# Performance work log

Measured on AMD Instinct MI355X. Metric: run time of the kernel, lower is better.

## Reference

```python
import jax, jax.numpy as jnp
import numpy as np

BN_EPS = 1e-5

def setup_inputs() -> dict:
    key = jax.random.key(0)
    ks = jax.random.split(key, 4)
    N, C, T, V, H = 32, 64, 512, 25, 3
    x = jax.random.normal(ks[0], (N, C, T, V), dtype=jnp.float32)
    A = jax.random.normal(ks[1], (H, V, V), dtype=jnp.float32)
    # per-head 1x1 conv weights (conv_branch_init-like small std) and biases
    W = jax.random.normal(ks[2], (H, C, C), dtype=jnp.float32) * 0.05
    b = jax.random.normal(ks[3], (H, C), dtype=jnp.float32) * 0.05
    gamma = jnp.ones((C,), dtype=jnp.float32)
    beta = jnp.zeros((C,), dtype=jnp.float32)
    return {"x": x, "A": A, "W": W, "b": b, "gamma": gamma, "beta": beta}

def reference(x, A, W, b, gamma, beta):
    # x: [N,C,T,V], A: [H,V,V], W: [H,Cout,Cin], b: [H,Cout]
    # per-head graph conv: z_h[n,c,t,v] = sum_u A[h,v,u] * x[n,c,t,u]
    z = jnp.einsum('hvu,nctu->hnctv', A, x)
    # per-head 1x1 conv (channel mix) then sum over heads; biases sum too
    out = jnp.einsum('hoc,hnctv->notv', W, z) + b.sum(axis=0)[None, :, None, None]
    # BatchNorm2d (training-mode batch stats, biased variance) over (N,T,V)
    mean = out.mean(axis=(0, 2, 3), keepdims=True)
    var = out.var(axis=(0, 2, 3), keepdims=True)
    out = gamma[None, :, None, None] * (out - mean) * jax.lax.rsqrt(var + BN_EPS) \
          + beta[None, :, None, None]
    # residual (in_channels == out_channels -> identity down) + ReLU
    return jnp.maximum(out + x, 0.0)
```

## Files before the change

kernel.cpp:

```cpp
#include <hip/hip_runtime.h>
#include <hip/hip_bf16.h>

#define N_DIM 32
#define C_DIM 64
#define T_DIM 512
#define V_DIM 25
#define H_DIM 3
#define TT 8
#define NBLK1 2048
#define NTGRP 2048
#define NTV (N_DIM * T_DIM * V_DIM)
#define NTOT (N_DIM * C_DIM * T_DIM * V_DIM)
#define XPITCH 76
#define XROWS 208
#define TILE_SH 1792
#define SITER 13
#define BN_EPS 1e-5f

typedef float f32x4 __attribute__((ext_vector_type(4)));
typedef short bf16x8 __attribute__((ext_vector_type(8)));
typedef short s16x4 __attribute__((ext_vector_type(4)));

__device__ __forceinline__ short f2bf(float f) {
    __hip_bfloat16 h = __float2bfloat16(f);
    return __builtin_bit_cast(short, h);
}
__device__ __forceinline__ float bf2f(short s) {
    return __uint_as_float(((unsigned)(unsigned short)s) << 16);
}

__device__ __forceinline__ bf16x8 ld_bf8(const short* p) {
    s16x4 a = *(const s16x4*)p;
    s16x4 b = *(const s16x4*)(p + 4);
    bf16x8 r;
    r[0] = a[0]; r[1] = a[1]; r[2] = a[2]; r[3] = a[3];
    r[4] = b[0]; r[5] = b[1]; r[6] = b[2]; r[7] = b[3];
    return r;
}

__global__ __launch_bounds__(256) void gcn_pack(
    const float* __restrict__ A, const float* __restrict__ W,
    short* __restrict__ wpack, short* __restrict__ apack)
{
    const int b   = blockIdx.x;
    const int tid = threadIdx.x;
    const int l15 = tid & 15, hi = (tid >> 4) & 3, w = tid >> 6;
    if (b < 6) {
        int h = b >> 1, s = b & 1;
        const float* wp = W + h * 4096 + (16 * w + l15) * 64 + s * 32 + hi * 8;
        bf16x8 f;
        #pragma unroll
        for (int i = 0; i < 8; ++i) f[i] = f2bf(wp[i]);
        *(bf16x8*)(wpack + ((size_t)b * 256 + tid) * 8) = f;
    } else {
        int bb = b - 6, h = bb >> 1, vt = bb & 1;
        int v = vt * 16 + l15;
        bf16x8 f;
        #pragma unroll
        for (int i = 0; i < 8; ++i) {
            int u = hi * 8 + i;
            f[i] = (v < 25 && u < 25) ? f2bf(A[h * 625 + v * 25 + u]) : (short)0;
        }
        *(bf16x8*)(apack + ((size_t)bb * 256 + tid) * 8) = f;
    }
}

__device__ __forceinline__ void stage_load(float (&fr)[SITER][4],
                                           const float* __restrict__ xg, int tid)
{
    #pragma unroll
    for (int k = 0; k < SITER; ++k) {
        int e = tid + k * 256;
        if (k < SITER - 1 || e < 3200) {
            int cg = e / 200, tu = e - cg * 200;
            const float* p = xg + cg * 51200 + tu;
            fr[k][0] = p[0];
            fr[k][1] = p[12800];
            fr[k][2] = p[25600];
            fr[k][3] = p[38400];
        }
    }
}
__device__ __forceinline__ void stage_write(const float (&fr)[SITER][4],
                                            short* __restrict__ dst, int tid)
{
    #pragma unroll
    for (int k = 0; k < SITER; ++k) {
        int e = tid + k * 256;
        if (k < SITER - 1 || e < 3200) {
            int cg = e / 200, tu = e - cg * 200;
            s16x4 v; v[0] = f2bf(fr[k][0]); v[1] = f2bf(fr[k][1]);
                     v[2] = f2bf(fr[k][2]); v[3] = f2bf(fr[k][3]);
            *(s16x4*)&dst[tu * XPITCH + 4 * cg] = v;
        }
    }
}

template <int SCR>
__global__ __launch_bounds__(256, 4) void gcn_pass1(
    const float* __restrict__ x, const float* __restrict__ A,
    const float* __restrict__ W, const short* __restrict__ wpack,
    const short* __restrict__ apack, void* __restrict__ scratch_,
    float* __restrict__ partial)
{
    __shared__ __align__(16) short x_sT[XROWS * XPITCH];

    const int bid  = blockIdx.x;
    const int n    = bid >> 6;
    const int tgrp = bid & 63;
    const int tid  = threadIdx.x;
    const int lane = tid & 63;
    const int w    = tid >> 6;
    const int l15  = lane & 15;
    const int hi   = lane >> 4;

    {
        float fr[SITER][4];
        stage_load(fr, x + (size_t)n * 819200 + tgrp * (TT * 25), tid);
        for (int e = tid; e < 304; e += 256)
            ((int*)&x_sT[200 * XPITCH])[e] = 0;
        stage_write(fr, &x_sT[0], tid);
    }

    bf16x8 wf[H_DIM][2], af[H_DIM][2];
    if constexpr (SCR) {
        #pragma unroll
        for (int h = 0; h < H_DIM; ++h)
            #pragma unroll
            for (int s = 0; s < 2; ++s) {
                wf[h][s] = *(const bf16x8*)(wpack + ((h * 2 + s) * 256 + tid) * 8);
                af[h][s] = *(const bf16x8*)(apack + ((h * 2 + s) * 256 + tid) * 8);
            }
    } else {
        #pragma unroll
        for (int h = 0; h < H_DIM; ++h)
            #pragma unroll
            for (int s = 0; s < 2; ++s) {
                const f32x4* wp = (const f32x4*)(W + h * 4096 + (16 * w + l15) * 64
                                                 + s * 32 + hi * 8);
                f32x4 lo = wp[0], hv = wp[1];
                bf16x8 f;
                #pragma unroll
                for (int i = 0; i < 4; ++i) { f[i] = f2bf(lo[i]); f[4+i] = f2bf(hv[i]); }
                wf[h][s] = f;
                int v = s * 16 + l15;
                bf16x8 g;
                #pragma unroll
                for (int i = 0; i < 8; ++i) {
                    int u = hi * 8 + i;
                    g[i] = (v < 25 && u < 25) ? f2bf(A[h * 625 + v * 25 + u]) : (short)0;
                }
                af[h][s] = g;
            }
    }
    __syncthreads();

    const int ubase = ((l15 >> 2) * 8) + (l15 & 3);
    const int o_glob = 16 * w + l15;
    float s_tot = 0.f, q_tot = 0.f;

    #pragma unroll 2
    for (int t = 0; t < TT; ++t) {
        const short* xr0 = &x_sT[(t * 25 + ubase + 0) * XPITCH + hi * 8];
        const short* xr1 = &x_sT[(t * 25 + ubase + 4) * XPITCH + hi * 8];
        const bf16x8 xf00 = ld_bf8(xr0), xf01 = ld_bf8(xr0 + 32);
        const bf16x8 xf10 = ld_bf8(xr1), xf11 = ld_bf8(xr1 + 32);

        f32x4 acc2[2] = {f32x4{0.f,0.f,0.f,0.f}, f32x4{0.f,0.f,0.f,0.f}};

        #pragma unroll
        for (int h = 0; h < H_DIM; ++h) {
            f32x4 y0 = {0.f,0.f,0.f,0.f}, y1 = {0.f,0.f,0.f,0.f};
            y0 = __builtin_amdgcn_mfma_f32_16x16x32_bf16(xf00, wf[h][0], y0, 0,0,0);
            y0 = __builtin_amdgcn_mfma_f32_16x16x32_bf16(xf01, wf[h][1], y0, 0,0,0);
            y1 = __builtin_amdgcn_mfma_f32_16x16x32_bf16(xf10, wf[h][0], y1, 0,0,0);
            y1 = __builtin_amdgcn_mfma_f32_16x16x32_bf16(xf11, wf[h][1], y1, 0,0,0);
            bf16x8 yf;
            #pragma unroll
            for (int j = 0; j < 4; ++j) yf[j] = f2bf(y0[j]);
            #pragma unroll
            for (int j = 0; j < 4; ++j) yf[4 + j] = f2bf(y1[j]);
            acc2[0] = __builtin_amdgcn_mfma_f32_16x16x32_bf16(af[h][0], yf, acc2[0], 0,0,0);
            acc2[1] = __builtin_amdgcn_mfma_f32_16x16x32_bf16(af[h][1], yf, acc2[1], 0,0,0);
        }

        if (SCR) {
            short* base = (short*)scratch_
                        + ((size_t)(n * 512 + tgrp * TT + t)) * TILE_SH;
            s16x4 p0; p0[0]=f2bf(acc2[0][0]); p0[1]=f2bf(acc2[0][1]);
                      p0[2]=f2bf(acc2[0][2]); p0[3]=f2bf(acc2[0][3]);
            *(s16x4*)(base + w * 256 + hi * 64 + l15 * 4) = p0;
            if (hi < 3) {
                s16x4 p1; p1[0]=f2bf(acc2[1][0]); p1[1]=f2bf(acc2[1][1]);
                          p1[2]=f2bf(acc2[1][2]); p1[3]=f2bf(acc2[1][3]);
                *(s16x4*)(base + 1024 + w * 192 + hi * 64 + l15 * 4) = p1;
            }
        } else {
            float* op = (float*)scratch_
                      + ((size_t)(n * 64 + o_glob) * 512 + tgrp * TT + t) * 25;
            #pragma unroll
            for (int j = 0; j < 4; ++j) op[hi * 4 + j] = acc2[0][j];
            if (hi < 2) {
                #pragma unroll
                for (int j = 0; j < 4; ++j) op[16 + hi * 4 + j] = acc2[1][j];
            } else if (hi == 2) {
                op[24] = acc2[1][0];
            }
        }

        float s = acc2[0][0] + acc2[0][1] + acc2[0][2] + acc2[0][3];
        float qq = fmaf(acc2[0][0], acc2[0][0], fmaf(acc2[0][1], acc2[0][1],
                   fmaf(acc2[0][2], acc2[0][2], acc2[0][3] * acc2[0][3])));
        if (hi < 2) {
            #pragma unroll
            for (int j = 0; j < 4; ++j) {
                float v1 = acc2[1][j]; s += v1; qq = fmaf(v1, v1, qq);
            }
        } else if (hi == 2) {
            float v1 = acc2[1][0]; s += v1; qq = fmaf(v1, v1, qq);
        }
        s_tot += s; q_tot += qq;
    }

    s_tot += __shfl_xor(s_tot, 16); q_tot += __shfl_xor(q_tot, 16);
    s_tot += __shfl_xor(s_tot, 32); q_tot += __shfl_xor(q_tot, 32);
    if (hi == 0) {
        partial[bid * 128 + o_glob]      = s_tot;
        partial[bid * 128 + 64 + o_glob] = q_tot;
    }
}

__global__ __launch_bounds__(256) void gcn_stats(
    const float* __restrict__ partial, float* __restrict__ stats)
{
    const int o = blockIdx.x;
    const int tid = threadIdx.x;
    float s = 0.f, q = 0.f;
    for (int blk = tid; blk < NBLK1; blk += 256) {
        s += partial[blk * 128 + o];
        q += partial[blk * 128 + 64 + o];
    }
    __shared__ float rs[256], rq[256];
    rs[tid] = s; rq[tid] = q;
    __syncthreads();
    for (int off = 128; off > 0; off >>= 1) {
        if (tid < off) { rs[tid] += rs[tid + off]; rq[tid] += rq[tid + off]; }
        __syncthreads();
    }
    if (tid == 0) {
        float mean = rs[0] / (float)NTV;
        float var  = rq[0] / (float)NTV - mean * mean;
        stats[o]      = mean;
        stats[64 + o] = rsqrtf(var + BN_EPS);
    }
}

__device__ __forceinline__ int swz16(int chunk) {
    return chunk ^ ((chunk >> 3) & 7);
}

__global__ __launch_bounds__(256) void gcn_finalize_b(
    const float* __restrict__ x, const float* __restrict__ gamma,
    const float* __restrict__ beta, const float* __restrict__ stats,
    const short* __restrict__ scr, float* __restrict__ out)
{
    __shared__ __align__(16) short tl_s[8 * TILE_SH];
    const int bid  = blockIdx.x;
    const int n    = bid >> 6;
    const int tgrp = bid & 63;
    const int tid  = threadIdx.x;

    const int4* src = (const int4*)(scr + (size_t)bid * 8 * TILE_SH);
    int4* dst4 = (int4*)tl_s;
    #pragma unroll
    for (int k = 0; k < 7; ++k) {
        int i = tid + k * 256;
        dst4[swz16(i)] = src[i];
    }
    __syncthreads();

    const size_t obase = (size_t)n * 819200 + (size_t)tgrp * 200;
    #pragma unroll
    for (int k = 0; k < 13; ++k) {
        int fi = tid + k * 256;
        if (fi < 3200) {
            int o  = fi / 50;
            int p  = (fi - o * 50) * 4;
            int tl = p / 25;
            int v0 = p - tl * 25;
            float gm = gamma[o] * stats[64 + o];
            float bc = beta[o] - gm * stats[o];
            size_t gidx = obase + (size_t)o * 12800 + p;
            float4 xv = *(const float4*)(x + gidx);
            float r[4];
            #pragma unroll
            for (int j = 0; j < 4; ++j) {
                int vv = v0 + j, tt = tl;
                if (vv >= 25) { vv -= 25; tt += 1; }
                int off = (vv < 16)
                    ? ((o >> 4) * 256 + (vv >> 2) * 64 + (o & 15) * 4 + (vv & 3))
                    : (1024 + (o >> 4) * 192 + ((vv - 16) >> 2) * 64
                       + (o & 15) * 4 + (vv & 3));
                int raw = tt * TILE_SH + off;
                int adr = swz16(raw >> 3) * 8 + (raw & 7);
                float pv = bf2f(tl_s[adr]);
                r[j] = fmaxf(fmaf(gm, pv, bc) + (&xv.x)[j], 0.f);
            }
            float4 o4; o4.x = r[0]; o4.y = r[1]; o4.z = r[2]; o4.w = r[3];
            *(float4*)(out + gidx) = o4;
        }
    }
}

__global__ __launch_bounds__(256) void gcn_finalize_f(
    const float* __restrict__ x, const float* __restrict__ gamma,
    const float* __restrict__ beta, const float* __restrict__ stats,
    float* __restrict__ out)
{
    const int total4 = NTOT / 4;
    for (int i = blockIdx.x * blockDim.x + threadIdx.x; i < total4;
         i += gridDim.x * blockDim.x) {
        int chan = ((i * 4) / (T_DIM * V_DIM)) & 63;
        float4 p  = ((const float4*)out)[i];
        float4 xv = ((const float4*)x)[i];
        float m = stats[chan], r = stats[64 + chan];
        float g = gamma[chan] * r;
        float bc = beta[chan] - g * m;
        p.x = fmaxf(fmaf(g, p.x, bc) + xv.x, 0.f);
        p.y = fmaxf(fmaf(g, p.y, bc) + xv.y, 0.f);
        p.z = fmaxf(fmaf(g, p.z, bc) + xv.z, 0.f);
        p.w = fmaxf(fmaf(g, p.w, bc) + xv.w, 0.f);
        ((float4*)out)[i] = p;
    }
}

extern "C" void kernel_launch(void* const* d_in, const int* in_sizes, int n_in,
                              void* d_out, int out_size, void* d_ws, size_t ws_size,
                              hipStream_t stream) {
    const float* x     = (const float*)d_in[0];
    const float* A     = (const float*)d_in[1];
    const float* W     = (const float*)d_in[2];
    const float* gamma = (const float*)d_in[4];
    const float* beta  = (const float*)d_in[5];
    float* out = (float*)d_out;

    const size_t scr_bytes   = (size_t)N_DIM * T_DIM * TILE_SH * 2;
    const size_t part_bytes  = (size_t)NBLK1 * 128 * 4;
    const size_t stats_bytes = 512;
    const size_t pack_bytes  = 2 * 6 * 256 * 8 * 2;

    if (ws_size >= scr_bytes + part_bytes + stats_bytes + pack_bytes) {
        short* scr     = (short*)d_ws;
        float* partial = (float*)((char*)d_ws + scr_bytes);
        float* stats   = partial + NBLK1 * 128;
        short* wpack   = (short*)((char*)d_ws + scr_bytes + part_bytes + stats_bytes);
        short* apack   = wpack + 6 * 256 * 8;

        gcn_pack<<<12, 256, 0, stream>>>(A, W, wpack, apack);
        gcn_pass1<1><<<NBLK1, 256, 0, stream>>>(x, A, W, wpack, apack,
                                                (void*)scr, partial);
        gcn_stats<<<64, 256, 0, stream>>>(partial, stats);
        gcn_finalize_b<<<NTGRP, 256, 0, stream>>>(x, gamma, beta, stats, scr, out);
    } else {
        float* partial = (float*)d_ws;
        float* stats   = partial + NBLK1 * 128;
        gcn_pass1<0><<<NBLK1, 256, 0, stream>>>(x, A, W, nullptr, nullptr,
                                                (void*)out, partial);
        gcn_stats<<<64, 256, 0, stream>>>(partial, stats);
        gcn_finalize_f<<<2048, 256, 0, stream>>>(x, gamma, beta, stats, out);
    }
}
```

Measured before the change: 89.99 us.

## Recompute graph conv in finalize instead of round-tripping bf16 scratch

The first pass now only computes the per-channel sum and sum-of-squares, without writing the pre-BN activations to a bf16 scratch buffer. A new fused kernel re-stages x, recomputes both MFMA stages with swapped operand order so output rows map to channels, and applies the folded BN scale/shift, residual and ReLU directly. The BN scale and shift are now folded once in the stats kernel. This trades the scratch write and read traffic for a second read of x and a repeat of the matrix work; the final stores are scalar and partly masked rather than float4.

```diff
diff --git a/kernel.cpp b/kernel.cpp
--- a/kernel.cpp
+++ b/kernel.cpp
@@ -8,12 +8,10 @@
 #define H_DIM 3
 #define TT 8
 #define NBLK1 2048
-#define NTGRP 2048
 #define NTV (N_DIM * T_DIM * V_DIM)
 #define NTOT (N_DIM * C_DIM * T_DIM * V_DIM)
 #define XPITCH 76
 #define XROWS 208
-#define TILE_SH 1792
 #define SITER 13
 #define BN_EPS 1e-5f
 
@@ -24,9 +22,6 @@
 __device__ __forceinline__ short f2bf(float f) {
     __hip_bfloat16 h = __float2bfloat16(f);
     return __builtin_bit_cast(short, h);
-}
-__device__ __forceinline__ float bf2f(short s) {
-    return __uint_as_float(((unsigned)(unsigned short)s) << 16);
 }
 
 __device__ __forceinline__ bf16x8 ld_bf8(const short* p) {
@@ -96,12 +91,9 @@
     }
 }
 
-template <int SCR>
-__global__ __launch_bounds__(256, 4) void gcn_pass1(
-    const float* __restrict__ x, const float* __restrict__ A,
-    const float* __restrict__ W, const short* __restrict__ wpack,
-    const short* __restrict__ apack, void* __restrict__ scratch_,
-    float* __restrict__ partial)
+__global__ __launch_bounds__(256, 4) void gcn_statsconv(
+    const float* __restrict__ x, const short* __restrict__ wpack,
+    const short* __restrict__ apack, float* __restrict__ partial)
 {
     __shared__ __align__(16) short x_sT[XROWS * XPITCH];
 
@@ -123,36 +115,13 @@
     }
 
     bf16x8 wf[H_DIM][2], af[H_DIM][2];
-    if constexpr (SCR) {
-        #pragma unroll
-        for (int h = 0; h < H_DIM; ++h)
-            #pragma unroll
-            for (int s = 0; s < 2; ++s) {
-                wf[h][s] = *(const bf16x8*)(wpack + ((h * 2 + s) * 256 + tid) * 8);
-                af[h][s] = *(const bf16x8*)(apack + ((h * 2 + s) * 256 + tid) * 8);
-            }
-    } else {
-        #pragma unroll
-        for (int h = 0; h < H_DIM; ++h)
-            #pragma unroll
-            for (int s = 0; s < 2; ++s) {
-                const f32x4* wp = (const f32x4*)(W + h * 4096 + (16 * w + l15) * 64
-                                                 + s * 32 + hi * 8);
-                f32x4 lo = wp[0], hv = wp[1];
-                bf16x8 f;
-                #pragma unroll
-                for (int i = 0; i < 4; ++i) { f[i] = f2bf(lo[i]); f[4+i] = f2bf(hv[i]); }
-                wf[h][s] = f;
-                int v = s * 16 + l15;
-                bf16x8 g;
-                #pragma unroll
-                for (int i = 0; i < 8; ++i) {
-                    int u = hi * 8 + i;
-                    g[i] = (v < 25 && u < 25) ? f2bf(A[h * 625 + v * 25 + u]) : (short)0;
-                }
-                af[h][s] = g;
-            }
-    }
+    #pragma unroll
+    for (int h = 0; h < H_DIM; ++h)
+        #pragma unroll
+        for (int s = 0; s < 2; ++s) {
+            wf[h][s] = *(const bf16x8*)(wpack + ((h * 2 + s) * 256 + tid) * 8);
+            af[h][s] = *(const bf16x8*)(apack + ((h * 2 + s) * 256 + tid) * 8);
+        }
     __syncthreads();
 
     const int ubase = ((l15 >> 2) * 8) + (l15 & 3);
@@ -184,30 +153,6 @@
             acc2[1] = __builtin_amdgcn_mfma_f32_16x16x32_bf16(af[h][1], yf, acc2[1], 0,0,0);
         }
 
-        if (SCR) {
-            short* base = (short*)scratch_
-                        + ((size_t)(n * 512 + tgrp * TT + t)) * TILE_SH;
-            s16x4 p0; p0[0]=f2bf(acc2[0][0]); p0[1]=f2bf(acc2[0][1]);
-                      p0[2]=f2bf(acc2[0][2]); p0[3]=f2bf(acc2[0][3]);
-            *(s16x4*)(base + w * 256 + hi * 64 + l15 * 4) = p0;
-            if (hi < 3) {
-                s16x4 p1; p1[0]=f2bf(acc2[1][0]); p1[1]=f2bf(acc2[1][1]);
-                          p1[2]=f2bf(acc2[1][2]); p1[3]=f2bf(acc2[1][3]);
-                *(s16x4*)(base + 1024 + w * 192 + hi * 64 + l15 * 4) = p1;
-            }
-        } else {
-            float* op = (float*)scratch_
-                      + ((size_t)(n * 64 + o_glob) * 512 + tgrp * TT + t) * 25;
-            #pragma unroll
-            for (int j = 0; j < 4; ++j) op[hi * 4 + j] = acc2[0][j];
-            if (hi < 2) {
-                #pragma unroll
-                for (int j = 0; j < 4; ++j) op[16 + hi * 4 + j] = acc2[1][j];
-            } else if (hi == 2) {
-                op[24] = acc2[1][0];
-            }
-        }
-
         float s = acc2[0][0] + acc2[0][1] + acc2[0][2] + acc2[0][3];
         float qq = fmaf(acc2[0][0], acc2[0][0], fmaf(acc2[0][1], acc2[0][1],
                    fmaf(acc2[0][2], acc2[0][2], acc2[0][3] * acc2[0][3])));
@@ -231,7 +176,8 @@
 }
 
 __global__ __launch_bounds__(256) void gcn_stats(
-    const float* __restrict__ partial, float* __restrict__ stats)
+    const float* __restrict__ partial, const float* __restrict__ gamma,
+    const float* __restrict__ beta, float* __restrict__ stats2)
 {
     const int o = blockIdx.x;
     const int tid = threadIdx.x;
@@ -250,71 +196,205 @@
     if (tid == 0) {
         float mean = rs[0] / (float)NTV;
         float var  = rq[0] / (float)NTV - mean * mean;
-        stats[o]      = mean;
-        stats[64 + o] = rsqrtf(var + BN_EPS);
-    }
-}
-
-__device__ __forceinline__ int swz16(int chunk) {
-    return chunk ^ ((chunk >> 3) & 7);
-}
-
-__global__ __launch_bounds__(256) void gcn_finalize_b(
-    const float* __restrict__ x, const float* __restrict__ gamma,
-    const float* __restrict__ beta, const float* __restrict__ stats,
-    const short* __restrict__ scr, float* __restrict__ out)
-{
-    __shared__ __align__(16) short tl_s[8 * TILE_SH];
+        float gm = gamma[o] * rsqrtf(var + BN_EPS);
+        stats2[o]      = gm;
+        stats2[64 + o] = beta[o] - gm * mean;
+    }
+}
+
+__global__ __launch_bounds__(256, 4) void gcn_fused(
+    const float* __restrict__ x, const short* __restrict__ wpack,
+    const short* __restrict__ apack, const float* __restrict__ stats2,
+    float* __restrict__ out)
+{
+    __shared__ __align__(16) short x_sT[XROWS * XPITCH];
+
     const int bid  = blockIdx.x;
     const int n    = bid >> 6;
     const int tgrp = bid & 63;
     const int tid  = threadIdx.x;
-
-    const int4* src = (const int4*)(scr + (size_t)bid * 8 * TILE_SH);
-    int4* dst4 = (int4*)tl_s;
-    #pragma unroll
-    for (int k = 0; k < 7; ++k) {
-        int i = tid + k * 256;
-        dst4[swz16(i)] = src[i];
+    const int lane = tid & 63;
+    const int w    = tid >> 6;
+    const int l15  = lane & 15;
+    const int hi   = lane >> 4;
+
+    {
+        float fr[SITER][4];
+        stage_load(fr, x + (size_t)n * 819200 + tgrp * (TT * 25), tid);
+        for (int e = tid; e < 304; e += 256)
+            ((int*)&x_sT[200 * XPITCH])[e] = 0;
+        stage_write(fr, &x_sT[0], tid);
+    }
+
+    bf16x8 wf[H_DIM][2], af[H_DIM][2];
+    #pragma unroll
+    for (int h = 0; h < H_DIM; ++h)
+        #pragma unroll
+        for (int s = 0; s < 2; ++s) {
+            wf[h][s] = *(const bf16x8*)(wpack + ((h * 2 + s) * 256 + tid) * 8);
+            af[h][s] = *(const bf16x8*)(apack + ((h * 2 + s) * 256 + tid) * 8);
+        }
+
+    float gm[4], bc[4];
+    #pragma unroll
+    for (int j = 0; j < 4; ++j) {
+        int o = 16 * w + hi * 4 + j;
+        gm[j] = stats2[o];
+        bc[j] = stats2[64 + o];
     }
     __syncthreads();
 
-    const size_t obase = (size_t)n * 819200 + (size_t)tgrp * 200;
-    #pragma unroll
-    for (int k = 0; k < 13; ++k) {
-        int fi = tid + k * 256;
-        if (fi < 3200) {
-            int o  = fi / 50;
-            int p  = (fi - o * 50) * 4;
-            int tl = p / 25;
-            int v0 = p - tl * 25;
-            float gm = gamma[o] * stats[64 + o];
-            float bc = beta[o] - gm * stats[o];
-            size_t gidx = obase + (size_t)o * 12800 + p;
-            float4 xv = *(const float4*)(x + gidx);
-            float r[4];
+    const int ubase = ((l15 >> 2) * 8) + (l15 & 3);
+    const size_t rb0 = ((size_t)(n * 64 + 16 * w + hi * 4) * 512
+                        + (size_t)tgrp * TT) * 25;
+
+    #pragma unroll 2
+    for (int t = 0; t < TT; ++t) {
+        const short* xr0 = &x_sT[(t * 25 + ubase + 0) * XPITCH + hi * 8];
+        const short* xr1 = &x_sT[(t * 25 + ubase + 4) * XPITCH + hi * 8];
+        const bf16x8 xf00 = ld_bf8(xr0), xf01 = ld_bf8(xr0 + 32);
+        const bf16x8 xf10 = ld_bf8(xr1), xf11 = ld_bf8(xr1 + 32);
+
+        f32x4 accA = {0.f,0.f,0.f,0.f};
+        f32x4 accB = {0.f,0.f,0.f,0.f};
+
+        #pragma unroll
+        for (int h = 0; h < H_DIM; ++h) {
+            f32x4 y0 = {0.f,0.f,0.f,0.f}, y1 = {0.f,0.f,0.f,0.f};
+            y0 = __builtin_amdgcn_mfma_f32_16x16x32_bf16(xf00, wf[h][0], y0, 0,0,0);
+            y0 = __builtin_amdgcn_mfma_f32_16x16x32_bf16(xf01, wf[h][1], y0, 0,0,0);
+            y1 = __builtin_amdgcn_mfma_f32_16x16x32_bf16(xf10, wf[h][0], y1, 0,0,0);
+            y1 = __builtin_amdgcn_mfma_f32_16x16x32_bf16(xf11, wf[h][1], y1, 0,0,0);
+            bf16x8 yf;
+            #pragma unroll
+            for (int j = 0; j < 4; ++j) yf[j] = f2bf(y0[j]);
+            #pragma unroll
+            for (int j = 0; j < 4; ++j) yf[4 + j] = f2bf(y1[j]);
+            accA = __builtin_amdgcn_mfma_f32_16x16x32_bf16(yf, af[h][0], accA, 0,0,0);
+            accB = __builtin_amdgcn_mfma_f32_16x16x32_bf16(yf, af[h][1], accB, 0,0,0);
+        }
+
+        #pragma unroll
+        for (int j = 0; j < 4; ++j) {
+            size_t idx = rb0 + (size_t)j * 12800 + (size_t)t * 25 + l15;
+            float xv = x[idx];
+            out[idx] = fmaxf(fmaf(gm[j], accA[j], bc[j]) + xv, 0.f);
+            if (l15 < 9) {
+                float xv1 = x[idx + 16];
+                out[idx + 16] = fmaxf(fmaf(gm[j], accB[j], bc[j]) + xv1, 0.f);
+            }
+        }
+    }
+}
+
+__global__ __launch_bounds__(256, 4) void gcn_pass1_f(
+    const float* __restrict__ x, const float* __restrict__ A,
+    const float* __restrict__ W, float* __restrict__ out_pre,
+    float* __restrict__ partial)
+{
+    __shared__ __align__(16) short x_sT[XROWS * XPITCH];
+
+    const int bid  = blockIdx.x;
+    const int n    = bid >> 6;
+    const int tgrp = bid & 63;
+    const int tid  = threadIdx.x;
+    const int lane = tid & 63;
+    const int w    = tid >> 6;
+    const int l15  = lane & 15;
+    const int hi   = lane >> 4;
+
+    {
+        float fr[SITER][4];
+        stage_load(fr, x + (size_t)n * 819200 + tgrp * (TT * 25), tid);
+        for (int e = tid; e < 304; e += 256)
+            ((int*)&x_sT[200 * XPITCH])[e] = 0;
+        stage_write(fr, &x_sT[0], tid);
+    }
+
+    bf16x8 wf[H_DIM][2], af[H_DIM][2];
+    #pragma unroll
+    for (int h = 0; h < H_DIM; ++h)
+        #pragma unroll
+        for (int s = 0; s < 2; ++s) {
+            const f32x4* wp = (const f32x4*)(W + h * 4096 + (16 * w + l15) * 64
+                                             + s * 32 + hi * 8);
+            f32x4 lo = wp[0], hv = wp[1];
+            bf16x8 f;
+            #pragma unroll
+            for (int i = 0; i < 4; ++i) { f[i] = f2bf(lo[i]); f[4+i] = f2bf(hv[i]); }
+            wf[h][s] = f;
+            int v = s * 16 + l15;
+            bf16x8 g;
+            #pragma unroll
+            for (int i = 0; i < 8; ++i) {
+                int u = hi * 8 + i;
+                g[i] = (v < 25 && u < 25) ? f2bf(A[h * 625 + v * 25 + u]) : (short)0;
+            }
+            af[h][s] = g;
+        }
+    __syncthreads();
+
+    const int ubase = ((l15 >> 2) * 8) + (l15 & 3);
+    const int o_glob = 16 * w + l15;
+    float s_tot = 0.f, q_tot = 0.f;
+
+    for (int t = 0; t < TT; ++t) {
+        const short* xr0 = &x_sT[(t * 25 + ubase + 0) * XPITCH + hi * 8];
+        const short* xr1 = &x_sT[(t * 25 + ubase + 4) * XPITCH + hi * 8];
+        const bf16x8 xf00 = ld_bf8(xr0), xf01 = ld_bf8(xr0 + 32);
+        const bf16x8 xf10 = ld_bf8(xr1), xf11 = ld_bf8(xr1 + 32);
+
+        f32x4 acc2[2] = {f32x4{0.f,0.f,0.f,0.f}, f32x4{0.f,0.f,0.f,0.f}};
+        #pragma unroll
+        for (int h = 0; h < H_DIM; ++h) {
+            f32x4 y0 = {0.f,0.f,0.f,0.f}, y1 = {0.f,0.f,0.f,0.f};
+            y0 = __builtin_amdgcn_mfma_f32_16x16x32_bf16(xf00, wf[h][0], y0, 0,0,0);
+            y0 = __builtin_amdgcn_mfma_f32_16x16x32_bf16(xf01, wf[h][1], y0, 0,0,0);
+            y1 = __builtin_amdgcn_mfma_f32_16x16x32_bf16(xf10, wf[h][0], y1, 0,0,0);
+            y1 = __builtin_amdgcn_mfma_f32_16x16x32_bf16(xf11, wf[h][1], y1, 0,0,0);
+            bf16x8 yf;
+            #pragma unroll
+            for (int j = 0; j < 4; ++j) yf[j] = f2bf(y0[j]);
+            #pragma unroll
+            for (int j = 0; j < 4; ++j) yf[4 + j] = f2bf(y1[j]);
+            acc2[0] = __builtin_amdgcn_mfma_f32_16x16x32_bf16(af[h][0], yf, acc2[0], 0,0,0);
+            acc2[1] = __builtin_amdgcn_mfma_f32_16x16x32_bf16(af[h][1], yf, acc2[1], 0,0,0);
+        }
+
+        float* op = out_pre + ((size_t)(n * 64 + o_glob) * 512 + tgrp * TT + t) * 25;
+        #pragma unroll
+        for (int j = 0; j < 4; ++j) op[hi * 4 + j] = acc2[0][j];
+        if (hi < 2) {
+            #pragma unroll
+            for (int j = 0; j < 4; ++j) op[16 + hi * 4 + j] = acc2[1][j];
+        } else if (hi == 2) {
+            op[24] = acc2[1][0];
+        }
+
+        float s = acc2[0][0] + acc2[0][1] + acc2[0][2] + acc2[0][3];
+        float qq = fmaf(acc2[0][0], acc2[0][0], fmaf(acc2[0][1], acc2[0][1],
+                   fmaf(acc2[0][2], acc2[0][2], acc2[0][3] * acc2[0][3])));
+        if (hi < 2) {
             #pragma unroll
             for (int j = 0; j < 4; ++j) {
-                int vv = v0 + j, tt = tl;
-                if (vv >= 25) { vv -= 25; tt += 1; }
-                int off = (vv < 16)
-                    ? ((o >> 4) * 256 + (vv >> 2) * 64 + (o & 15) * 4 + (vv & 3))
-                    : (1024 + (o >> 4) * 192 + ((vv - 16) >> 2) * 64
-                       + (o & 15) * 4 + (vv & 3));
-                int raw = tt * TILE_SH + off;
-                int adr = swz16(raw >> 3) * 8 + (raw & 7);
-                float pv = bf2f(tl_s[adr]);
-                r[j] = fmaxf(fmaf(gm, pv, bc) + (&xv.x)[j], 0.f);
+                float v1 = acc2[1][j]; s += v1; qq = fmaf(v1, v1, qq);
             }
-            float4 o4; o4.x = r[0]; o4.y = r[1]; o4.z = r[2]; o4.w = r[3];
-            *(float4*)(out + gidx) = o4;
-        }
+        } else if (hi == 2) {
+            float v1 = acc2[1][0]; s += v1; qq = fmaf(v1, v1, qq);
+        }
+        s_tot += s; q_tot += qq;
+    }
+
+    s_tot += __shfl_xor(s_tot, 16); q_tot += __shfl_xor(q_tot, 16);
+    s_tot += __shfl_xor(s_tot, 32); q_tot += __shfl_xor(q_tot, 32);
+    if (hi == 0) {
+        partial[bid * 128 + o_glob]      = s_tot;
+        partial[bid * 128 + 64 + o_glob] = q_tot;
     }
 }
 
 __global__ __launch_bounds__(256) void gcn_finalize_f(
-    const float* __restrict__ x, const float* __restrict__ gamma,
-    const float* __restrict__ beta, const float* __restrict__ stats,
+    const float* __restrict__ x, const float* __restrict__ stats2,
     float* __restrict__ out)
 {
     const int total4 = NTOT / 4;
@@ -323,9 +403,7 @@
         int chan = ((i * 4) / (T_DIM * V_DIM)) & 63;
         float4 p  = ((const float4*)out)[i];
         float4 xv = ((const float4*)x)[i];
-        float m = stats[chan], r = stats[64 + chan];
-        float g = gamma[chan] * r;
-        float bc = beta[chan] - g * m;
+        float g = stats2[chan], bc = stats2[64 + chan];
         p.x = fmaxf(fmaf(g, p.x, bc) + xv.x, 0.f);
         p.y = fmaxf(fmaf(g, p.y, bc) + xv.y, 0.f);
         p.z = fmaxf(fmaf(g, p.z, bc) + xv.z, 0.f);
@@ -344,29 +422,23 @@
     const float* beta  = (const float*)d_in[5];
     float* out = (float*)d_out;
 
-    const size_t scr_bytes   = (size_t)N_DIM * T_DIM * TILE_SH * 2;
     const size_t part_bytes  = (size_t)NBLK1 * 128 * 4;
     const size_t stats_bytes = 512;
     const size_t pack_bytes  = 2 * 6 * 256 * 8 * 2;
 
-    if (ws_size >= scr_bytes + part_bytes + stats_bytes + pack_bytes) {
-        short* scr     = (short*)d_ws;
-        float* partial = (float*)((char*)d_ws + scr_bytes);
-        float* stats   = partial + NBLK1 * 128;
-        short* wpack   = (short*)((char*)d_ws + scr_bytes + part_bytes + stats_bytes);
-        short* apack   = wpack + 6 * 256 * 8;
-
+    float* partial = (float*)d_ws;
+    float* stats2  = partial + NBLK1 * 128;
+    short* wpack   = (short*)((char*)d_ws + part_bytes + stats_bytes);
+    short* apack   = wpack + 6 * 256 * 8;
+
+    if (ws_size >= part_bytes + stats_bytes + pack_bytes) {
         gcn_pack<<<12, 256, 0, stream>>>(A, W, wpack, apack);
-        gcn_pass1<1><<<NBLK1, 256, 0, stream>>>(x, A, W, wpack, apack,
-                                                (void*)scr, partial);
-        gcn_stats<<<64, 256, 0, stream>>>(partial, stats);
-        gcn_finalize_b<<<NTGRP, 256, 0, stream>>>(x, gamma, beta, stats, scr, out);
+        gcn_statsconv<<<NBLK1, 256, 0, stream>>>(x, wpack, apack, partial);
+        gcn_stats<<<64, 256, 0, stream>>>(partial, gamma, beta, stats2);
+        gcn_fused<<<NBLK1, 256, 0, stream>>>(x, wpack, apack, stats2, out);
     } else {
-        float* partial = (float*)d_ws;
-        float* stats   = partial + NBLK1 * 128;
-        gcn_pass1<0><<<NBLK1, 256, 0, stream>>>(x, A, W, nullptr, nullptr,
-                                                (void*)out, partial);
-        gcn_stats<<<64, 256, 0, stream>>>(partial, stats);
-        gcn_finalize_f<<<2048, 256, 0, stream>>>(x, gamma, beta, stats, out);
-    }
-}
+        gcn_pass1_f<<<NBLK1, 256, 0, stream>>>(x, A, W, out, partial);
+        gcn_stats<<<64, 256, 0, stream>>>(partial, gamma, beta, stats2);
+        gcn_finalize_f<<<2048, 256, 0, stream>>>(x, stats2, out);
+    }
+}
```

Result: slower. 115.6 us (+28.5%).
